# Kernel optimization log

Measured on AMD Instinct MI355X. Metric: run time of the kernel, lower is better.

The kernel has to match this reference:

```python
import jax, jax.numpy as jnp
import numpy as np

WINDOW_SIZE = 11
SIGMA = 1.5
VAL_RANGE = 1.0
C1 = (0.01 * VAL_RANGE) ** 2
C2 = (0.03 * VAL_RANGE) ** 2


def _gaussian_window(channel):
    # 1D gaussian -> 2D separable window, replicated per channel (depthwise)
    x = np.arange(WINDOW_SIZE) - WINDOW_SIZE // 2
    g = np.exp(-(x.astype(np.float64) ** 2) / (2.0 * SIGMA ** 2))
    g = g / g.sum()
    w2 = np.outer(g, g).astype(np.float32)  # [K,K]
    w = np.broadcast_to(w2, (channel, 1, WINDOW_SIZE, WINDOW_SIZE)).copy()
    return jnp.asarray(w)


def _dwconv(x, w):
    # depthwise conv2d, SAME-style padding K//2, groups = channels
    pad = WINDOW_SIZE // 2
    return jax.lax.conv_general_dilated(
        x, w, window_strides=(1, 1),
        padding=[(pad, pad), (pad, pad)],
        dimension_numbers=('NCHW', 'OIHW', 'NCHW'),
        feature_group_count=x.shape[1],
    )


def setup_inputs() -> dict:
    key = jax.random.key(0)
    k1, k2 = jax.random.split(key)
    img1 = jax.random.uniform(k1, (16, 3, 512, 512), dtype=jnp.float32)
    img2 = jax.random.uniform(k2, (16, 3, 512, 512), dtype=jnp.float32)
    return {"img1": img1, "img2": img2}


def reference(img1, img2):
    channel = img1.shape[1]
    w = _gaussian_window(channel).astype(img1.dtype)

    mu1 = _dwconv(img1, w)
    mu2 = _dwconv(img2, w)
    mu1_sq = mu1 * mu1
    mu2_sq = mu2 * mu2
    mu1_mu2 = mu1 * mu2

    sigma1_sq = _dwconv(img1 * img1, w) - mu1_sq
    sigma2_sq = _dwconv(img2 * img2, w) - mu2_sq
    sigma12 = _dwconv(img1 * img2, w) - mu1_mu2

    v1 = 2.0 * sigma12 + C2
    v2 = sigma1_sq + sigma2_sq + C2 + 1e-06

    ssim_map = (2.0 * mu1_mu2 + C1) * v1 / ((mu1_sq + mu2_sq + C1) * v2)
    return jnp.mean(ssim_map)
```

## Files before the change

kernel.cpp:

```cpp
#include <hip/hip_runtime.h>
#include <math.h>

#define IMG_H 512
#define IMG_W 512
#define NPLANES 48
#define TX 64
#define TY 32
#define VW 74
#define VSTRIDE 75
#define NF 5
#define BLOCK 256

template <bool BORDER>
__device__ __forceinline__ void vpass(const float* __restrict__ i1,
                                      const float* __restrict__ i2,
                                      float* __restrict__ vs,
                                      const float* w,
                                      int x0, int y0, int tid) {
    for (int t = tid; t < VW * (TY / 4); t += BLOCK) {
        int r0 = (t / VW) * 4;
        int c  = t - (t / VW) * VW;
        int gx = x0 - 5 + c;
        float acc[NF][4];
        #pragma unroll
        for (int f = 0; f < NF; ++f)
            #pragma unroll
            for (int j = 0; j < 4; ++j) acc[f][j] = 0.f;

        #pragma unroll
        for (int i = 0; i < 14; ++i) {
            int gy = y0 + r0 - 5 + i;
            float a, b;
            if (BORDER) {
                bool ok = ((unsigned)gy < IMG_H) & ((unsigned)gx < IMG_W);
                int g = ok ? gy * IMG_W + gx : 0;
                a = i1[g]; b = i2[g];
                a = ok ? a : 0.f;
                b = ok ? b : 0.f;
            } else {
                int g = gy * IMG_W + gx;
                a = i1[g]; b = i2[g];
            }
            float aa = a * a, bb = b * b, ab = a * b;
            #pragma unroll
            for (int j = 0; j < 4; ++j) {
                int k = i - j;
                if (k >= 0 && k < 11) {
                    float wk = w[k];
                    acc[0][j] += wk * a;
                    acc[1][j] += wk * b;
                    acc[2][j] += wk * aa;
                    acc[3][j] += wk * bb;
                    acc[4][j] += wk * ab;
                }
            }
        }
        #pragma unroll
        for (int f = 0; f < NF; ++f)
            #pragma unroll
            for (int j = 0; j < 4; ++j)
                vs[f * TY * VSTRIDE + (r0 + j) * VSTRIDE + c] = acc[f][j];
    }
}

__global__ __launch_bounds__(BLOCK, 3)
void ssim_main(const float* __restrict__ img1, const float* __restrict__ img2,
               float* __restrict__ blocksums) {
    __shared__ float vs[NF * TY * VSTRIDE];
    __shared__ float red[4];

    const int tid = threadIdx.x;
    const int x0 = blockIdx.x * TX;
    const int y0 = blockIdx.y * TY;
    const float* i1 = img1 + (size_t)blockIdx.z * (IMG_H * IMG_W);
    const float* i2 = img2 + (size_t)blockIdx.z * (IMG_H * IMG_W);

    float w[11];
    {
        float t[11], s = 0.f;
        #pragma unroll
        for (int i = 0; i < 11; ++i) {
            float d = (float)(i - 5);
            t[i] = expf(-d * d / 4.5f);
            s += t[i];
        }
        #pragma unroll
        for (int i = 0; i < 11; ++i) w[i] = t[i] / s;
    }

    bool border = (blockIdx.x == 0) | (blockIdx.x == gridDim.x - 1) |
                  (blockIdx.y == 0) | (blockIdx.y == gridDim.y - 1);
    if (border) vpass<true >(i1, i2, vs, w, x0, y0, tid);
    else        vpass<false>(i1, i2, vs, w, x0, y0, tid);
    __syncthreads();

    float lsum = 0.f;
    for (int t = tid; t < TY * 16; t += BLOCK) {
        int r  = t >> 4;
        int c0 = (t & 15) << 2;
        float acc[NF][4];
        #pragma unroll
        for (int f = 0; f < NF; ++f) {
            const float* vp = &vs[f * TY * VSTRIDE + r * VSTRIDE + c0];
            float hv[14];
            #pragma unroll
            for (int i = 0; i < 14; ++i) hv[i] = vp[i];
            #pragma unroll
            for (int j = 0; j < 4; ++j) {
                float s = 0.f;
                #pragma unroll
                for (int k = 0; k < 11; ++k) s += w[k] * hv[k + j];
                acc[f][j] = s;
            }
        }
        #pragma unroll
        for (int j = 0; j < 4; ++j) {
            float mu1 = acc[0][j], mu2 = acc[1][j];
            float ex2 = acc[2][j], ey2 = acc[3][j], exy = acc[4][j];
            float mu1s = mu1 * mu1;
            float mu2s = mu2 * mu2;
            float mu12 = mu1 * mu2;
            float s1q = ex2 - mu1s;
            float s2q = ey2 - mu2s;
            float s12 = exy - mu12;
            float v1 = 2.f * s12 + 9e-4f;
            float v2 = s1q + s2q + 9.01e-4f;
            float num = (2.f * mu12 + 1e-4f) * v1;
            float den = (mu1s + mu2s + 1e-4f) * v2;
            lsum += num / den;
        }
    }

    #pragma unroll
    for (int off = 32; off; off >>= 1) lsum += __shfl_down(lsum, off, 64);
    if ((tid & 63) == 0) red[tid >> 6] = lsum;
    __syncthreads();
    if (tid == 0) {
        float bs = red[0] + red[1] + red[2] + red[3];
        int bid = (blockIdx.z * gridDim.y + blockIdx.y) * gridDim.x + blockIdx.x;
        blocksums[bid] = bs;
    }
}

__global__ void ssim_finalize(const float* __restrict__ bs, float* __restrict__ out, int n) {
    __shared__ double red[4];
    double s = 0.0;
    for (int i = threadIdx.x; i < n; i += BLOCK) s += (double)bs[i];
    #pragma unroll
    for (int off = 32; off; off >>= 1) s += __shfl_down(s, off, 64);
    if ((threadIdx.x & 63) == 0) red[threadIdx.x >> 6] = s;
    __syncthreads();
    if (threadIdx.x == 0)
        out[0] = (float)((red[0] + red[1] + red[2] + red[3]) / 12582912.0);
}

extern "C" void kernel_launch(void* const* d_in, const int* in_sizes, int n_in,
                              void* d_out, int out_size, void* d_ws, size_t ws_size,
                              hipStream_t stream) {
    const float* img1 = (const float*)d_in[0];
    const float* img2 = (const float*)d_in[1];
    float* out = (float*)d_out;
    float* bsums = (float*)d_ws;

    dim3 grid(IMG_W / TX, IMG_H / TY, NPLANES);
    ssim_main<<<grid, BLOCK, 0, stream>>>(img1, img2, bsums);
    ssim_finalize<<<1, BLOCK, 0, stream>>>(bsums, out, 6144);
}
```

Baseline: 179.7 us.

## Process tile in two halves with smaller LDS, constexpr weights and fast reciprocal

Each block now processes its 64x32 tile as two 16-row halves that reuse a half-size shared buffer. This lowers LDS usage so the launch bound can raise occupancy to 6 blocks. Gaussian weights become compile-time constants instead of per-thread expf, and the final division uses a hardware reciprocal. The cost is re-reading the 10-row vertical halo for each half, extra barriers, and slightly reduced division precision.

```diff
diff --git a/kernel.cpp b/kernel.cpp
--- a/kernel.cpp
+++ b/kernel.cpp
@@ -1,57 +1,64 @@
 #include <hip/hip_runtime.h>
-#include <math.h>
 
 #define IMG_H 512
 #define IMG_W 512
 #define NPLANES 48
 #define TX 64
-#define TY 32
+#define TY 16
 #define VW 74
 #define VSTRIDE 75
 #define NF 5
 #define BLOCK 256
 
+static constexpr float WG[11] = {
+    0.0010283804f, 0.0075987582f, 0.0360007723f, 0.1093606901f,
+    0.2130055377f, 0.2660117259f, 0.2130055377f, 0.1093606901f,
+    0.0360007723f, 0.0075987582f, 0.0010283804f
+};
+
 template <bool BORDER>
 __device__ __forceinline__ void vpass(const float* __restrict__ i1,
                                       const float* __restrict__ i2,
                                       float* __restrict__ vs,
-                                      const float* w,
                                       int x0, int y0, int tid) {
     for (int t = tid; t < VW * (TY / 4); t += BLOCK) {
-        int r0 = (t / VW) * 4;
-        int c  = t - (t / VW) * VW;
+        int rq = t / VW;
+        int c  = t - rq * VW;
+        int r0 = rq << 2;
         int gx = x0 - 5 + c;
+        int gy0 = y0 + r0 - 5;
         float acc[NF][4];
         #pragma unroll
         for (int f = 0; f < NF; ++f)
             #pragma unroll
             for (int j = 0; j < 4; ++j) acc[f][j] = 0.f;
 
+        const float* p1 = i1 + (ptrdiff_t)gy0 * IMG_W + gx;
+        const float* p2 = i2 + (ptrdiff_t)gy0 * IMG_W + gx;
         #pragma unroll
         for (int i = 0; i < 14; ++i) {
-            int gy = y0 + r0 - 5 + i;
             float a, b;
             if (BORDER) {
+                int gy = gy0 + i;
                 bool ok = ((unsigned)gy < IMG_H) & ((unsigned)gx < IMG_W);
                 int g = ok ? gy * IMG_W + gx : 0;
                 a = i1[g]; b = i2[g];
                 a = ok ? a : 0.f;
                 b = ok ? b : 0.f;
             } else {
-                int g = gy * IMG_W + gx;
-                a = i1[g]; b = i2[g];
+                a = p1[(ptrdiff_t)i * IMG_W];
+                b = p2[(ptrdiff_t)i * IMG_W];
             }
             float aa = a * a, bb = b * b, ab = a * b;
             #pragma unroll
             for (int j = 0; j < 4; ++j) {
                 int k = i - j;
                 if (k >= 0 && k < 11) {
-                    float wk = w[k];
-                    acc[0][j] += wk * a;
-                    acc[1][j] += wk * b;
-                    acc[2][j] += wk * aa;
-                    acc[3][j] += wk * bb;
-                    acc[4][j] += wk * ab;
+                    acc[0][j] += WG[k] * a;
+                    acc[1][j] += WG[k] * b;
+                    acc[2][j] += WG[k] * aa;
+                    acc[3][j] += WG[k] * bb;
+                    acc[4][j] += WG[k] * ab;
                 }
             }
         }
@@ -63,7 +70,45 @@
     }
 }
 
-__global__ __launch_bounds__(BLOCK, 3)
+__device__ __forceinline__ float hpass_ssim(const float* __restrict__ vs, int tid) {
+    int r  = tid >> 4;
+    int c0 = (tid & 15) << 2;
+    float acc[NF][4];
+    #pragma unroll
+    for (int f = 0; f < NF; ++f) {
+        const float* vp = vs + f * TY * VSTRIDE + r * VSTRIDE + c0;
+        float hv[14];
+        #pragma unroll
+        for (int i = 0; i < 14; ++i) hv[i] = vp[i];
+        #pragma unroll
+        for (int j = 0; j < 4; ++j) {
+            float s = 0.f;
+            #pragma unroll
+            for (int k = 0; k < 11; ++k) s += WG[k] * hv[k + j];
+            acc[f][j] = s;
+        }
+    }
+    float lsum = 0.f;
+    #pragma unroll
+    for (int j = 0; j < 4; ++j) {
+        float mu1 = acc[0][j], mu2 = acc[1][j];
+        float ex2 = acc[2][j], ey2 = acc[3][j], exy = acc[4][j];
+        float mu1s = mu1 * mu1;
+        float mu2s = mu2 * mu2;
+        float mu12 = mu1 * mu2;
+        float s1q = ex2 - mu1s;
+        float s2q = ey2 - mu2s;
+        float s12 = exy - mu12;
+        float v1 = 2.f * s12 + 9e-4f;
+        float v2 = s1q + s2q + 9.01e-4f;
+        float num = (2.f * mu12 + 1e-4f) * v1;
+        float den = (mu1s + mu2s + 1e-4f) * v2;
+        lsum += num * __builtin_amdgcn_rcpf(den);
+    }
+    return lsum;
+}
+
+__global__ __launch_bounds__(BLOCK, 6)
 void ssim_main(const float* __restrict__ img1, const float* __restrict__ img2,
                float* __restrict__ blocksums) {
     __shared__ float vs[NF * TY * VSTRIDE];
@@ -71,64 +116,20 @@
 
     const int tid = threadIdx.x;
     const int x0 = blockIdx.x * TX;
-    const int y0 = blockIdx.y * TY;
     const float* i1 = img1 + (size_t)blockIdx.z * (IMG_H * IMG_W);
     const float* i2 = img2 + (size_t)blockIdx.z * (IMG_H * IMG_W);
-
-    float w[11];
-    {
-        float t[11], s = 0.f;
-        #pragma unroll
-        for (int i = 0; i < 11; ++i) {
-            float d = (float)(i - 5);
-            t[i] = expf(-d * d / 4.5f);
-            s += t[i];
-        }
-        #pragma unroll
-        for (int i = 0; i < 11; ++i) w[i] = t[i] / s;
-    }
-
-    bool border = (blockIdx.x == 0) | (blockIdx.x == gridDim.x - 1) |
-                  (blockIdx.y == 0) | (blockIdx.y == gridDim.y - 1);
-    if (border) vpass<true >(i1, i2, vs, w, x0, y0, tid);
-    else        vpass<false>(i1, i2, vs, w, x0, y0, tid);
-    __syncthreads();
+    const bool xb = (blockIdx.x == 0) | (blockIdx.x == gridDim.x - 1);
 
     float lsum = 0.f;
-    for (int t = tid; t < TY * 16; t += BLOCK) {
-        int r  = t >> 4;
-        int c0 = (t & 15) << 2;
-        float acc[NF][4];
-        #pragma unroll
-        for (int f = 0; f < NF; ++f) {
-            const float* vp = &vs[f * TY * VSTRIDE + r * VSTRIDE + c0];
-            float hv[14];
-            #pragma unroll
-            for (int i = 0; i < 14; ++i) hv[i] = vp[i];
-            #pragma unroll
-            for (int j = 0; j < 4; ++j) {
-                float s = 0.f;
-                #pragma unroll
-                for (int k = 0; k < 11; ++k) s += w[k] * hv[k + j];
-                acc[f][j] = s;
-            }
-        }
-        #pragma unroll
-        for (int j = 0; j < 4; ++j) {
-            float mu1 = acc[0][j], mu2 = acc[1][j];
-            float ex2 = acc[2][j], ey2 = acc[3][j], exy = acc[4][j];
-            float mu1s = mu1 * mu1;
-            float mu2s = mu2 * mu2;
-            float mu12 = mu1 * mu2;
-            float s1q = ex2 - mu1s;
-            float s2q = ey2 - mu2s;
-            float s12 = exy - mu12;
-            float v1 = 2.f * s12 + 9e-4f;
-            float v2 = s1q + s2q + 9.01e-4f;
-            float num = (2.f * mu12 + 1e-4f) * v1;
-            float den = (mu1s + mu2s + 1e-4f) * v2;
-            lsum += num / den;
-        }
+    for (int half = 0; half < 2; ++half) {
+        int y0 = blockIdx.y * 32 + half * TY;
+        bool border = xb | (half == 0 ? (blockIdx.y == 0)
+                                      : (blockIdx.y == gridDim.y - 1));
+        if (border) vpass<true >(i1, i2, vs, x0, y0, tid);
+        else        vpass<false>(i1, i2, vs, x0, y0, tid);
+        __syncthreads();
+        lsum += hpass_ssim(vs, tid);
+        __syncthreads();
     }
 
     #pragma unroll
@@ -162,7 +163,7 @@
     float* out = (float*)d_out;
     float* bsums = (float*)d_ws;
 
-    dim3 grid(IMG_W / TX, IMG_H / TY, NPLANES);
+    dim3 grid(IMG_W / TX, IMG_H / 32, NPLANES);
     ssim_main<<<grid, BLOCK, 0, stream>>>(img1, img2, bsums);
     ssim_finalize<<<1, BLOCK, 0, stream>>>(bsums, out, 6144);
 }
```

After: 235.6 us. 1.31x slower.
